# Performance work log

Measured on AMD Instinct MI355X. Metric: run time of the kernel, lower is better.

Reference implementation:

```python
import jax, jax.numpy as jnp
import numpy as np

V, BLOCK, E, H = 50257, 2048, 256, 8
DH = E // H  # head_size = 32
B, T = 2, 2048
SCALE = 1.0 / np.float32(np.sqrt(DH))


def setup_inputs() -> dict:
    key = jax.random.key(0)
    ks = jax.random.split(key, 9)
    s = 0.02
    return {
        "idx": jax.random.randint(ks[0], (B, T), 0, V),
        "targets": jax.random.randint(ks[1], (B, T), 0, V),
        "tok_emb": jax.random.normal(ks[2], (V, E), jnp.float32) * s,
        "pos_emb": jax.random.normal(ks[3], (BLOCK, E), jnp.float32) * s,
        "Wq": jax.random.normal(ks[4], (H, E, DH), jnp.float32) * s,
        "Wk": jax.random.normal(ks[5], (H, E, DH), jnp.float32) * s,
        "Wv": jax.random.normal(ks[6], (H, E, DH), jnp.float32) * s,
        "Wlm": jax.random.normal(ks[7], (V, E), jnp.float32) * s,
        "blm": jnp.zeros((V,), jnp.float32),
    }


def reference(idx, targets, tok_emb, pos_emb, Wq, Wk, Wv, Wlm, blm):
    t = idx.shape[1]
    x = tok_emb[idx] + pos_emb[:t]  # [B,T,E]
    # all heads batched (original loops over heads; same math)
    q = jnp.einsum('bte,hed->bhtd', x, Wq)
    k = jnp.einsum('bte,hed->bhtd', x, Wk)
    v = jnp.einsum('bte,hed->bhtd', x, Wv)
    scores = jnp.einsum('bhqd,bhkd->bhqk', q, k) * SCALE  # [B,H,T,T]
    causal = jnp.tril(jnp.ones((t, t), dtype=bool))
    # faithful to original: tril then masked_fill(scores == 0, -inf)
    scores = jnp.where(causal, scores, 0.0)
    scores = jnp.where(scores == 0.0, -jnp.inf, scores)
    # faithful to original bug: softmax over the QUERY axis (torch dim=1 of [b,t,t])
    attn = jax.nn.softmax(scores, axis=2)
    out = jnp.einsum('bhqk,bhkd->bqhd', attn, v).reshape(idx.shape[0], t, E)  # concat heads
    logits = out @ Wlm.T + blm  # [B,T,V]
    logp = jax.nn.log_softmax(logits, axis=-1)
    loss = -jnp.take_along_axis(logp, targets[..., None], axis=-1).mean()
    return logits, loss
```

## Files before the change

### kernel.cpp

```cpp
#include <hip/hip_runtime.h>
#include <hip/hip_bf16.h>
#include <cstdint>
#include <cstddef>

typedef __bf16 bf16x8 __attribute__((ext_vector_type(8)));
typedef __bf16 bf16x4 __attribute__((ext_vector_type(4)));
typedef float  f32x4  __attribute__((ext_vector_type(4)));
typedef float  f32x16 __attribute__((ext_vector_type(16)));

#define SCALE_QK 0.17677669529663687f
#define V_SIZE 50257
#define T_SEQ  2048
#define E_DIM  256
#define NROWS  4096
#define LNB    786
#define NPAD   (LNB * 64)

__device__ __forceinline__ f32x4 mfma16(bf16x8 a, bf16x8 b, f32x4 c) {
    return __builtin_amdgcn_mfma_f32_16x16x32_bf16(a, b, c, 0, 0, 0);
}
__device__ __forceinline__ f32x16 mfma32(bf16x8 a, bf16x8 b, f32x16 c) {
    return __builtin_amdgcn_mfma_f32_32x32x16_bf16(a, b, c, 0, 0, 0);
}

#define GLOAD_LDS16(gptr, lptr) \
    __builtin_amdgcn_global_load_lds((const __attribute__((address_space(1))) void*)(gptr), \
                                     (__attribute__((address_space(3))) void*)(lptr), 16, 0, 0)

#define PREP_EMBED 1024
#define PREP_WQKV  (PREP_EMBED + 768)
#define PREP_CVT   (PREP_WQKV + 12576)
#define PREP_ZERO  (PREP_CVT + 128)
__global__ void __launch_bounds__(256)
k_prep(const int* __restrict__ idx, const float* __restrict__ tok,
       const float* __restrict__ pos, __bf16* __restrict__ X,
       const float* __restrict__ Wq, const float* __restrict__ Wk,
       const float* __restrict__ Wv, __bf16* __restrict__ Wo,
       const float* __restrict__ Wlm, __bf16* __restrict__ WlmB,
       float* __restrict__ Dcol) {
    const int bx = blockIdx.x, tid = threadIdx.x;
    if (bx < PREP_EMBED) {
        int row = bx * 4 + (tid >> 6);
        int tl = row & (T_SEQ - 1);
        int tk = idx[row];
        int e = (tid & 63) * 4;
        f32x4 a = *(const f32x4*)(tok + (size_t)tk * E_DIM + e);
        f32x4 p = *(const f32x4*)(pos + (size_t)tl * E_DIM + e);
        bf16x4 o;
#pragma unroll
        for (int i = 0; i < 4; ++i) o[i] = (__bf16)(a[i] + p[i]);
        *(bf16x4*)(X + (size_t)row * E_DIM + e) = o;
    } else if (bx < PREP_WQKV) {
        int n = bx - PREP_EMBED;
        int sel = n >> 8, hd = n & 255, h = hd >> 5, d = hd & 31;
        const float* W = (sel == 0) ? Wq : (sel == 1) ? Wk : Wv;
        Wo[(size_t)n * E_DIM + tid] = (__bf16)W[((size_t)h * E_DIM + tid) * 32 + d];
    } else if (bx < PREP_CVT) {
        size_t i = ((size_t)(bx - PREP_WQKV) * 256 + tid) * 4;
        bf16x4 o = {};
        if (i + 4 <= (size_t)V_SIZE * E_DIM) {
            f32x4 v = *(const f32x4*)(Wlm + i);
#pragma unroll
            for (int j = 0; j < 4; ++j) o[j] = (__bf16)v[j];
        }
        *(bf16x4*)(WlmB + i) = o;
    } else {
        Dcol[(bx - PREP_CVT) * 256 + tid] = 0.f;
    }
}

template <int KK>
__global__ void __launch_bounds__(256, 4)
k_gemm_bt(const __bf16* __restrict__ A, const __bf16* __restrict__ B,
          __bf16* __restrict__ Cout, int N) {
    __shared__ __align__(16) __bf16 Alds[128 * 64];
    __shared__ __align__(16) __bf16 Blds[128 * 64];

    const int tid = threadIdx.x;
    const int lane = tid & 63, w = tid >> 6;
    const int wr = w >> 1, wc = w & 1;
    const int brow = blockIdx.x * 128, bcol = blockIdx.y * 128;
    const int gg = lane >> 4, li = lane & 15;

    f32x4 acc[4][4] = {};

#pragma unroll
    for (int t = 0; t < KK / 64; ++t) {
#pragma unroll
        for (int i = 0; i < 4; ++i) {
            int cb = (w * 4 + i) * 64;
            int c = cb + lane;
            int r = c >> 3, kbs = (c & 7) ^ (r & 7);
            GLOAD_LDS16(A + (size_t)(brow + r) * KK + t * 64 + kbs * 8, (char*)Alds + cb * 16);
            GLOAD_LDS16(B + (size_t)(bcol + r) * KK + t * 64 + kbs * 8, (char*)Blds + cb * 16);
        }
        __syncthreads();
#pragma unroll
        for (int ks = 0; ks < 2; ++ks) {
            bf16x8 af[4], bfr[4];
#pragma unroll
            for (int mi = 0; mi < 4; ++mi) {
                int r = wr * 64 + mi * 16 + li;
                int kbyte = (ks * 64 + gg * 16) ^ ((r & 7) << 4);
                af[mi] = *(const bf16x8*)((const char*)Alds + r * 128 + kbyte);
            }
#pragma unroll
            for (int ni = 0; ni < 4; ++ni) {
                int r = wc * 64 + ni * 16 + li;
                int kbyte = (ks * 64 + gg * 16) ^ ((r & 7) << 4);
                bfr[ni] = *(const bf16x8*)((const char*)Blds + r * 128 + kbyte);
            }
#pragma unroll
            for (int mi = 0; mi < 4; ++mi)
#pragma unroll
                for (int ni = 0; ni < 4; ++ni)
                    acc[mi][ni] = mfma16(bfr[ni], af[mi], acc[mi][ni]);
        }
        if (t + 1 < KK / 64) __syncthreads();
    }
#pragma unroll
    for (int mi = 0; mi < 4; ++mi) {
        const size_t mrow = (size_t)(brow + wr * 64 + mi * 16 + li) * N;
#pragma unroll
        for (int ni = 0; ni < 4; ++ni) {
            int nc = wc * 64 + ni * 16 + gg * 4;
            f32x4 v = acc[mi][ni];
            bf16x4 o;
#pragma unroll
            for (int j = 0; j < 4; ++j) o[j] = (__bf16)v[j];
            *(bf16x4*)(Cout + mrow + bcol + nc) = o;
        }
    }
}

__global__ void __launch_bounds__(256, 4)
k_logits(const __bf16* __restrict__ A, const __bf16* __restrict__ B,
         float* __restrict__ C, const float* __restrict__ bias,
         float* __restrict__ partials) {
    __shared__ __align__(16) __bf16 Alds[256 * 64];
    __shared__ __align__(16) __bf16 Blds[64 * 64];
    __shared__ __align__(16) float bias_lds[64];

    const int tid = threadIdx.x, lane = tid & 63, w = tid >> 6;
    const int brow = blockIdx.x * 256, bcol = blockIdx.y * 64;
    const int gg = lane >> 4, li = lane & 15;

    if (tid < 64) bias_lds[tid] = (bcol + tid < V_SIZE) ? bias[bcol + tid] : 0.f;

    f32x4 acc[4][4] = {};

#pragma unroll
    for (int t = 0; t < 4; ++t) {
#pragma unroll
        for (int i = 0; i < 8; ++i) {
            int cb = (w * 8 + i) * 64;
            int c = cb + lane;
            int r = c >> 3, kbs = (c & 7) ^ (r & 7);
            GLOAD_LDS16(A + (size_t)(brow + r) * E_DIM + t * 64 + kbs * 8, (char*)Alds + cb * 16);
        }
#pragma unroll
        for (int i = 0; i < 2; ++i) {
            int cb = (w * 2 + i) * 64;
            int c = cb + lane;
            int r = c >> 3, kbs = (c & 7) ^ (r & 7);
            GLOAD_LDS16(B + (size_t)(bcol + r) * E_DIM + t * 64 + kbs * 8, (char*)Blds + cb * 16);
        }
        __syncthreads();
#pragma unroll
        for (int ks = 0; ks < 2; ++ks) {
            bf16x8 af[4], bfr[4];
#pragma unroll
            for (int mi = 0; mi < 4; ++mi) {
                int r = w * 64 + mi * 16 + li;
                int kbyte = (ks * 64 + gg * 16) ^ ((r & 7) << 4);
                af[mi] = *(const bf16x8*)((const char*)Alds + r * 128 + kbyte);
            }
#pragma unroll
            for (int ni = 0; ni < 4; ++ni) {
                int r = ni * 16 + li;
                int kbyte = (ks * 64 + gg * 16) ^ ((r & 7) << 4);
                bfr[ni] = *(const bf16x8*)((const char*)Blds + r * 128 + kbyte);
            }
#pragma unroll
            for (int mi = 0; mi < 4; ++mi)
#pragma unroll
                for (int ni = 0; ni < 4; ++ni)
                    acc[mi][ni] = mfma16(bfr[ni], af[mi], acc[mi][ni]);
        }
        if (t < 3) __syncthreads();
    }

    if (bcol + 64 <= V_SIZE) {
#pragma unroll
        for (int mi = 0; mi < 4; ++mi) {
            const size_t mrow = (size_t)(brow + w * 64 + mi * 16 + li) * V_SIZE;
            float s = 0.f;
#pragma unroll
            for (int ni = 0; ni < 4; ++ni) {
                int nc = ni * 16 + gg * 4;
                f32x4 v = acc[mi][ni];
                f32x4 bv = *(const f32x4*)&bias_lds[nc];
#pragma unroll
                for (int j = 0; j < 4; ++j) { v[j] += bv[j]; s += __expf(v[j]); }
                *(f32x4*)(C + mrow + bcol + nc) = v;
            }
            s += __shfl_xor(s, 16); s += __shfl_xor(s, 32);
            if (gg == 0)
                partials[(size_t)blockIdx.y * NROWS + brow + w * 64 + mi * 16 + li] = s;
        }
    } else {
#pragma unroll
        for (int mi = 0; mi < 4; ++mi) {
            const size_t mrow = (size_t)(brow + w * 64 + mi * 16 + li) * V_SIZE;
            float s = 0.f;
#pragma unroll
            for (int ni = 0; ni < 4; ++ni) {
                int nc = ni * 16 + gg * 4;
#pragma unroll
                for (int j = 0; j < 4; ++j) {
                    int col = bcol + nc + j;
                    if (col < V_SIZE) {
                        float v = acc[mi][ni][j] + bias_lds[nc + j];
                        s += __expf(v);
                        C[mrow + col] = v;
                    }
                }
            }
            s += __shfl_xor(s, 16); s += __shfl_xor(s, 32);
            if (gg == 0)
                partials[(size_t)blockIdx.y * NROWS + brow + w * 64 + mi * 16 + li] = s;
        }
    }
}

__global__ void __launch_bounds__(256)
k_pass1(const __bf16* __restrict__ QKV, float* __restrict__ Dcol) {
    int p = blockIdx.x;
    int kt = 0;
    while (p >= 16 - kt) { p -= 16 - kt; ++kt; }
    const int qc = kt + p;
    const int bh = blockIdx.y;
    const int b = bh >> 3, h = bh & 7;
    const int tid = threadIdx.x, lane = tid & 63, w = tid >> 6;
    const int g = lane >> 5, li = lane & 31;
    __shared__ __align__(16) __bf16 Klds[4 * 128 * 8];
    __shared__ __align__(16) __bf16 Qlds[4 * 128 * 8];

    const size_t baseQ = ((size_t)b * T_SEQ) * 768 + h * 32;
    const size_t baseK = baseQ + 256;

#pragma unroll
    for (int i = 0; i < 2; ++i) {
        int c = i * 256 + tid; int k = c >> 2, db = c & 3;
        *(bf16x8*)(Klds + (db * 128 + k) * 8) =
            *(const bf16x8*)(QKV + baseK + (size_t)(kt * 128 + k) * 768 + db * 8);
        *(bf16x8*)(Qlds + (db * 128 + k) * 8) =
            *(const bf16x8*)(QKV + baseQ + (size_t)(qc * 128 + k) * 768 + db * 8);
    }
    __syncthreads();

    float csum = 0.f;
    const int kglob = kt * 128 + w * 32 + li;
#pragma unroll
    for (int qs = 0; qs < 4; ++qs) {
        f32x16 sacc = {};
#pragma unroll
        for (int ks = 0; ks < 2; ++ks) {
            bf16x8 aq = *(const bf16x8*)(Qlds + ((ks * 2 + g) * 128 + qs * 32 + li) * 8);
            bf16x8 bk = *(const bf16x8*)(Klds + ((ks * 2 + g) * 128 + w * 32 + li) * 8);
            sacc = mfma32(aq, bk, sacc);
        }
#pragma unroll
        for (int r = 0; r < 16; ++r) {
            int qrow = qc * 128 + qs * 32 + ((r & 3) + 8 * (r >> 2) + 4 * g);
            if (kglob <= qrow) csum += __expf(sacc[r] * SCALE_QK);
        }
    }
    csum += __shfl_xor(csum, 32);
    if (g == 0) atomicAdd(&Dcol[(size_t)bh * T_SEQ + kglob], csum);
}

__global__ void __launch_bounds__(256)
k_pass2(const __bf16* __restrict__ QKV, const float* __restrict__ Dcol,
        float* __restrict__ Yf0, float* __restrict__ Yf1) {
    const int p = blockIdx.x, bh = blockIdx.y;
    const int pi = p >> 1, par = p & 1;
    const int b = bh >> 3, h = bh & 7;
    const int tid = threadIdx.x, lane = tid & 63, w = tid >> 6;
    const int g = lane >> 5, li = lane & 31;
    float* __restrict__ Yf = par ? Yf1 : Yf0;
    __shared__ __align__(16) __bf16 Qlds[4 * 128 * 8];
    __shared__ __align__(16) __bf16 Klds[4 * 128 * 8];
    __shared__ __align__(16) __bf16 UT[16 * 32 * 8];
    __shared__ __align__(16) __bf16 Plds[4][32 * 136];

    const size_t baseQ = ((size_t)b * T_SEQ) * 768 + h * 32;
    const size_t baseK = baseQ + 256;
    const size_t baseV = baseQ + 512;

#pragma unroll
    for (int ti = 0; ti < 2; ++ti) {
        const int qt = ti ? (15 - pi) : pi;
        __syncthreads();
#pragma unroll
        for (int i = 0; i < 2; ++i) {
            int c = i * 256 + tid; int q = c >> 2, db = c & 3;
            *(bf16x8*)(Qlds + (db * 128 + q) * 8) =
                *(const bf16x8*)(QKV + baseQ + (size_t)(qt * 128 + q) * 768 + db * 8);
        }
        f32x16 oacc = {};
        const int qrow = qt * 128 + w * 32 + li;

        for (int kc = par; kc <= qt; kc += 2) {
            __syncthreads();
#pragma unroll
            for (int i = 0; i < 2; ++i) {
                int c = i * 256 + tid; int k = c >> 2, db = c & 3;
                *(bf16x8*)(Klds + (db * 128 + k) * 8) =
                    *(const bf16x8*)(QKV + baseK + (size_t)(kc * 128 + k) * 768 + db * 8);
            }
#pragma unroll
            for (int i = 0; i < 4; ++i) {
                int c = i * 256 + tid; int k = c & 127, d4 = c >> 7;
                float rD = 1.0f / Dcol[(size_t)bh * T_SEQ + kc * 128 + k];
                bf16x4 v4 = *(const bf16x4*)(QKV + baseV + (size_t)(kc * 128 + k) * 768 + d4 * 4);
                int kb = k >> 3, j = k & 7;
#pragma unroll
                for (int t2 = 0; t2 < 4; ++t2)
                    UT[((size_t)kb * 32 + d4 * 4 + t2) * 8 + j] = (__bf16)((float)v4[t2] * rD);
            }
            __syncthreads();

#pragma unroll
            for (int ksub = 0; ksub < 4; ++ksub) {
                int kbase = kc * 128 + ksub * 32;
                f32x16 sacc = {};
#pragma unroll
                for (int ks = 0; ks < 2; ++ks) {
                    bf16x8 ak = *(const bf16x8*)(Klds + ((ks * 2 + g) * 128 + ksub * 32 + li) * 8);
                    bf16x8 bq = *(const bf16x8*)(Qlds + ((ks * 2 + g) * 128 + w * 32 + li) * 8);
                    sacc = mfma32(ak, bq, sacc);
                }
                float pv[16];
#pragma unroll
                for (int r = 0; r < 16; ++r) {
                    int kk = kbase + (r & 3) + 8 * (r >> 2) + 4 * g;
                    pv[r] = (kk <= qrow) ? __expf(sacc[r] * SCALE_QK) : 0.f;
                }
#pragma unroll
                for (int t2 = 0; t2 < 4; ++t2) {
                    bf16x4 pk;
#pragma unroll
                    for (int e = 0; e < 4; ++e) pk[e] = (__bf16)pv[4 * t2 + e];
                    *(bf16x4*)(&Plds[w][li * 136 + ksub * 32 + 8 * t2 + 4 * g]) = pk;
                }
            }
#pragma unroll
            for (int ks16 = 0; ks16 < 8; ++ks16) {
                bf16x8 ap = *(const bf16x8*)(&Plds[w][li * 136 + ks16 * 16 + g * 8]);
                bf16x8 bu = *(const bf16x8*)(UT + ((ks16 * 2 + g) * 32 + li) * 8);
                oacc = mfma32(ap, bu, oacc);
            }
        }
#pragma unroll
        for (int r = 0; r < 16; ++r) {
            int q = qt * 128 + w * 32 + (r & 3) + 8 * (r >> 2) + 4 * g;
            Yf[((size_t)b * T_SEQ + q) * E_DIM + h * 32 + li] = oacc[r];
        }
    }
}

__global__ void k_ycvt(const float* __restrict__ a, const float* __restrict__ b,
                       __bf16* __restrict__ y, int n4) {
    int i = blockIdx.x * 256 + threadIdx.x;
    if (i < n4) {
        f32x4 va = ((const f32x4*)a)[i], vb = ((const f32x4*)b)[i];
        bf16x4 o;
#pragma unroll
        for (int j = 0; j < 4; ++j) o[j] = (__bf16)(va[j] + vb[j]);
        ((bf16x4*)y)[i] = o;
    }
}

__global__ void k_rowlse(const float* __restrict__ partials, const float* __restrict__ logits,
                         const int* __restrict__ tgt, float* __restrict__ rowloss) {
    int r = blockIdx.x * 256 + threadIdx.x;
    float s = 0.f;
    for (int i = 0; i < LNB; ++i) s += partials[(size_t)i * NROWS + r];
    float lse = logf(s);
    rowloss[r] = lse - logits[(size_t)r * V_SIZE + tgt[r]];
}

__global__ void k_loss(const float* __restrict__ rowloss, float* __restrict__ out) {
    __shared__ float red[4];
    float s = 0.f;
    for (int i = threadIdx.x; i < NROWS; i += 256) s += rowloss[i];
    for (int m = 1; m < 64; m <<= 1) s += __shfl_xor(s, m);
    if ((threadIdx.x & 63) == 0) red[threadIdx.x >> 6] = s;
    __syncthreads();
    if (threadIdx.x == 0) out[0] = (red[0] + red[1] + red[2] + red[3]) / (float)NROWS;
}

extern "C" void kernel_launch(void* const* d_in, const int* in_sizes, int n_in,
                              void* d_out, int out_size, void* d_ws, size_t ws_size,
                              hipStream_t stream) {
    const int*   idx = (const int*)d_in[0];
    const int*   tgt = (const int*)d_in[1];
    const float* tok = (const float*)d_in[2];
    const float* pos = (const float*)d_in[3];
    const float* Wq  = (const float*)d_in[4];
    const float* Wk  = (const float*)d_in[5];
    const float* Wv  = (const float*)d_in[6];
    const float* Wlm = (const float*)d_in[7];
    const float* blm = (const float*)d_in[8];

    float* logits = (float*)d_out;
    float* loss   = logits + (size_t)NROWS * V_SIZE;

    char* ws = (char*)d_ws;
    __bf16* X        = (__bf16*)ws; ws += (size_t)NROWS * E_DIM * 2;
    __bf16* Wqkv     = (__bf16*)ws; ws += (size_t)768 * E_DIM * 2;
    __bf16* QKV      = (__bf16*)ws; ws += (size_t)NROWS * 768 * 2;
    float*  Dcol     = (float*)ws;  ws += (size_t)16 * T_SEQ * 4;
    __bf16* Y        = (__bf16*)ws; ws += (size_t)NROWS * E_DIM * 2;
    float*  Yf0      = (float*)ws;  ws += (size_t)NROWS * E_DIM * 4;
    float*  Yf1      = (float*)ws;  ws += (size_t)NROWS * E_DIM * 4;
    __bf16* WlmB     = (__bf16*)ws; ws += (size_t)NPAD * E_DIM * 2;
    float*  partials = (float*)ws;  ws += (size_t)LNB * NROWS * 4;
    float*  rowloss  = (float*)ws;  ws += (size_t)NROWS * 4;

    k_prep<<<PREP_ZERO, 256, 0, stream>>>(idx, tok, pos, X, Wq, Wk, Wv, Wqkv,
                                          Wlm, WlmB, Dcol);
    k_gemm_bt<E_DIM><<<dim3(NROWS / 128, 768 / 128), 256, 0, stream>>>(
        X, Wqkv, QKV, 768);
    k_pass1<<<dim3(136, 16), 256, 0, stream>>>(QKV, Dcol);
    k_pass2<<<dim3(16, 16), 256, 0, stream>>>(QKV, Dcol, Yf0, Yf1);
    k_ycvt<<<(NROWS * E_DIM / 4 + 255) / 256, 256, 0, stream>>>(Yf0, Yf1, Y, NROWS * E_DIM / 4);
    k_logits<<<dim3(NROWS / 256, LNB), 256, 0, stream>>>(
        Y, WlmB, logits, blm, partials);
    k_rowlse<<<NROWS / 256, 256, 0, stream>>>(partials, logits, tgt, rowloss);
    k_loss<<<1, 256, 0, stream>>>(rowloss, loss);
}
```

Measured before the change: 480.6 us.

## Retile LM-head logits GEMM to 128x128 and overlap epilogue with next tile's K-loop

The logits kernel changes from 256x64 tiles to 128x128 tiles with a 2x2 wave layout. Each block now walks four consecutive 128-column vocab tiles, double-buffering the accumulators so the previous tile's bias/exp/store epilogue runs interleaved with the next tile's loads and MFMAs. This aims to hide the large fp32 logits write and exp cost behind compute and to halve the partials array and its reduction. The cost is more registers (two accumulator sets), which may lower occupancy, plus extra LDS for per-wave sums and bias.

```diff
diff --git a/kernel.cpp b/kernel.cpp
--- a/kernel.cpp
+++ b/kernel.cpp
@@ -13,8 +13,8 @@
 #define T_SEQ  2048
 #define E_DIM  256
 #define NROWS  4096
-#define LNB    786
-#define NPAD   (LNB * 64)
+#define NNB    393
+#define NPAD   (NNB * 128)
 
 __device__ __forceinline__ f32x4 mfma16(bf16x8 a, bf16x8 b, f32x4 c) {
     return __builtin_amdgcn_mfma_f32_16x16x32_bf16(a, b, c, 0, 0, 0);
@@ -137,47 +137,41 @@
 k_logits(const __bf16* __restrict__ A, const __bf16* __restrict__ B,
          float* __restrict__ C, const float* __restrict__ bias,
          float* __restrict__ partials) {
-    __shared__ __align__(16) __bf16 Alds[256 * 64];
-    __shared__ __align__(16) __bf16 Blds[64 * 64];
-    __shared__ __align__(16) float bias_lds[64];
+    __shared__ __align__(16) __bf16 Alds[128 * 64];
+    __shared__ __align__(16) __bf16 Blds[128 * 64];
+    __shared__ __align__(16) float bias_lds[2][128];
+    __shared__ float wsum[2][128][2];
 
     const int tid = threadIdx.x, lane = tid & 63, w = tid >> 6;
-    const int brow = blockIdx.x * 256, bcol = blockIdx.y * 64;
-    const int gg = lane >> 4, li = lane & 15;
-
-    if (tid < 64) bias_lds[tid] = (bcol + tid < V_SIZE) ? bias[bcol + tid] : 0.f;
-
-    f32x4 acc[4][4] = {};
-
-#pragma unroll
-    for (int t = 0; t < 4; ++t) {
-#pragma unroll
-        for (int i = 0; i < 8; ++i) {
-            int cb = (w * 8 + i) * 64;
+    const int wr = w >> 1, wc = w & 1, gg = lane >> 4, li = lane & 15;
+    const int brow = blockIdx.x * 128;
+    const int base = blockIdx.y * 4;
+    const bool full4 = (base + 4 <= NNB);
+
+    auto stage = [&](int bn, int t) {
+#pragma unroll
+        for (int i = 0; i < 4; ++i) {
+            int cb = (w * 4 + i) * 64;
             int c = cb + lane;
             int r = c >> 3, kbs = (c & 7) ^ (r & 7);
             GLOAD_LDS16(A + (size_t)(brow + r) * E_DIM + t * 64 + kbs * 8, (char*)Alds + cb * 16);
-        }
-#pragma unroll
-        for (int i = 0; i < 2; ++i) {
-            int cb = (w * 2 + i) * 64;
-            int c = cb + lane;
-            int r = c >> 3, kbs = (c & 7) ^ (r & 7);
-            GLOAD_LDS16(B + (size_t)(bcol + r) * E_DIM + t * 64 + kbs * 8, (char*)Blds + cb * 16);
-        }
-        __syncthreads();
+            GLOAD_LDS16(B + (size_t)(bn * 128 + r) * E_DIM + t * 64 + kbs * 8, (char*)Blds + cb * 16);
+        }
+    };
+
+    auto compute = [&](f32x4 (&acc)[4][4]) {
 #pragma unroll
         for (int ks = 0; ks < 2; ++ks) {
             bf16x8 af[4], bfr[4];
 #pragma unroll
             for (int mi = 0; mi < 4; ++mi) {
-                int r = w * 64 + mi * 16 + li;
+                int r = wr * 64 + mi * 16 + li;
                 int kbyte = (ks * 64 + gg * 16) ^ ((r & 7) << 4);
                 af[mi] = *(const bf16x8*)((const char*)Alds + r * 128 + kbyte);
             }
 #pragma unroll
             for (int ni = 0; ni < 4; ++ni) {
-                int r = ni * 16 + li;
+                int r = wc * 64 + ni * 16 + li;
                 int kbyte = (ks * 64 + gg * 16) ^ ((r & 7) << 4);
                 bfr[ni] = *(const bf16x8*)((const char*)Blds + r * 128 + kbyte);
             }
@@ -187,49 +181,102 @@
                 for (int ni = 0; ni < 4; ++ni)
                     acc[mi][ni] = mfma16(bfr[ni], af[mi], acc[mi][ni]);
         }
-        if (t < 3) __syncthreads();
-    }
-
-    if (bcol + 64 <= V_SIZE) {
+    };
+
+    auto epislice = [&](const f32x4 (&acc)[4][4], int mi, int bn, int pb) {
+        const size_t mrow = (size_t)(brow + wr * 64 + mi * 16 + li) * V_SIZE;
+        const int bcol = bn * 128;
+        float s = 0.f;
+#pragma unroll
+        for (int ni = 0; ni < 4; ++ni) {
+            int nc = wc * 64 + ni * 16 + gg * 4;
+            f32x4 v = acc[mi][ni];
+            f32x4 bv = *(const f32x4*)&bias_lds[pb][nc];
+#pragma unroll
+            for (int j = 0; j < 4; ++j) { v[j] += bv[j]; s += __expf(v[j]); }
+            *(f32x4*)(C + mrow + bcol + nc) = v;
+        }
+        s += __shfl_xor(s, 16); s += __shfl_xor(s, 32);
+        if (gg == 0) wsum[pb][wr * 64 + mi * 16 + li][wc] = s;
+    };
+
+    auto kloop_ov = [&](f32x4 (&cur)[4][4], int bn, int pb,
+                        const f32x4 (&prev)[4][4], int pbn, int ppb) {
+#pragma unroll
+        for (int m2 = 0; m2 < 4; ++m2)
+#pragma unroll
+            for (int n2 = 0; n2 < 4; ++n2)
+                cur[m2][n2] = (f32x4){0.f, 0.f, 0.f, 0.f};
+        if (tid < 128) bias_lds[pb][tid] = bias[bn * 128 + tid];
+#pragma unroll
+        for (int t = 0; t < 4; ++t) {
+            stage(bn, t);
+            epislice(prev, t, pbn, ppb);
+            __syncthreads();
+            compute(cur);
+            __syncthreads();
+        }
+    };
+
+    if (full4) {
+        f32x4 a0[4][4] = {}, a1[4][4] = {};
+        if (tid < 128) bias_lds[0][tid] = bias[base * 128 + tid];
+#pragma unroll
+        for (int t = 0; t < 4; ++t) {
+            stage(base, t);
+            __syncthreads();
+            compute(a0);
+            __syncthreads();
+        }
+        kloop_ov(a1, base + 1, 1, a0, base + 0, 0);
+        if (tid < 128) partials[(size_t)(base + 0) * NROWS + brow + tid] =
+            wsum[0][tid][0] + wsum[0][tid][1];
+        kloop_ov(a0, base + 2, 0, a1, base + 1, 1);
+        if (tid < 128) partials[(size_t)(base + 1) * NROWS + brow + tid] =
+            wsum[1][tid][0] + wsum[1][tid][1];
+        kloop_ov(a1, base + 3, 1, a0, base + 2, 0);
+        if (tid < 128) partials[(size_t)(base + 2) * NROWS + brow + tid] =
+            wsum[0][tid][0] + wsum[0][tid][1];
+#pragma unroll
+        for (int mi = 0; mi < 4; ++mi) epislice(a1, mi, base + 3, 1);
+        __syncthreads();
+        if (tid < 128) partials[(size_t)(base + 3) * NROWS + brow + tid] =
+            wsum[1][tid][0] + wsum[1][tid][1];
+    } else {
+        const int bn = base;
+        const int bcol = bn * 128;
+        if (tid < 128) bias_lds[0][tid] = (bcol + tid < V_SIZE) ? bias[bcol + tid] : 0.f;
+        f32x4 a0[4][4] = {};
+#pragma unroll
+        for (int t = 0; t < 4; ++t) {
+            stage(bn, t);
+            __syncthreads();
+            compute(a0);
+            __syncthreads();
+        }
 #pragma unroll
         for (int mi = 0; mi < 4; ++mi) {
-            const size_t mrow = (size_t)(brow + w * 64 + mi * 16 + li) * V_SIZE;
+            const size_t mrow = (size_t)(brow + wr * 64 + mi * 16 + li) * V_SIZE;
             float s = 0.f;
 #pragma unroll
             for (int ni = 0; ni < 4; ++ni) {
-                int nc = ni * 16 + gg * 4;
-                f32x4 v = acc[mi][ni];
-                f32x4 bv = *(const f32x4*)&bias_lds[nc];
-#pragma unroll
-                for (int j = 0; j < 4; ++j) { v[j] += bv[j]; s += __expf(v[j]); }
-                *(f32x4*)(C + mrow + bcol + nc) = v;
-            }
-            s += __shfl_xor(s, 16); s += __shfl_xor(s, 32);
-            if (gg == 0)
-                partials[(size_t)blockIdx.y * NROWS + brow + w * 64 + mi * 16 + li] = s;
-        }
-    } else {
-#pragma unroll
-        for (int mi = 0; mi < 4; ++mi) {
-            const size_t mrow = (size_t)(brow + w * 64 + mi * 16 + li) * V_SIZE;
-            float s = 0.f;
-#pragma unroll
-            for (int ni = 0; ni < 4; ++ni) {
-                int nc = ni * 16 + gg * 4;
+                int nc = wc * 64 + ni * 16 + gg * 4;
 #pragma unroll
                 for (int j = 0; j < 4; ++j) {
                     int col = bcol + nc + j;
                     if (col < V_SIZE) {
-                        float v = acc[mi][ni][j] + bias_lds[nc + j];
+                        float v = a0[mi][ni][j] + bias_lds[0][nc + j];
                         s += __expf(v);
                         C[mrow + col] = v;
                     }
                 }
             }
             s += __shfl_xor(s, 16); s += __shfl_xor(s, 32);
-            if (gg == 0)
-                partials[(size_t)blockIdx.y * NROWS + brow + w * 64 + mi * 16 + li] = s;
-        }
+            if (gg == 0) wsum[0][wr * 64 + mi * 16 + li][wc] = s;
+        }
+        __syncthreads();
+        if (tid < 128)
+            partials[(size_t)bn * NROWS + brow + tid] = wsum[0][tid][0] + wsum[0][tid][1];
     }
 }
 
@@ -386,7 +433,7 @@
                          const int* __restrict__ tgt, float* __restrict__ rowloss) {
     int r = blockIdx.x * 256 + threadIdx.x;
     float s = 0.f;
-    for (int i = 0; i < LNB; ++i) s += partials[(size_t)i * NROWS + r];
+    for (int i = 0; i < NNB; ++i) s += partials[(size_t)i * NROWS + r];
     float lse = logf(s);
     rowloss[r] = lse - logits[(size_t)r * V_SIZE + tgt[r]];
 }
@@ -426,7 +473,7 @@
     float*  Yf0      = (float*)ws;  ws += (size_t)NROWS * E_DIM * 4;
     float*  Yf1      = (float*)ws;  ws += (size_t)NROWS * E_DIM * 4;
     __bf16* WlmB     = (__bf16*)ws; ws += (size_t)NPAD * E_DIM * 2;
-    float*  partials = (float*)ws;  ws += (size_t)LNB * NROWS * 4;
+    float*  partials = (float*)ws;  ws += (size_t)NNB * NROWS * 4;
     float*  rowloss  = (float*)ws;  ws += (size_t)NROWS * 4;
 
     k_prep<<<PREP_ZERO, 256, 0, stream>>>(idx, tok, pos, X, Wq, Wk, Wv, Wqkv,
@@ -436,7 +483,7 @@
     k_pass1<<<dim3(136, 16), 256, 0, stream>>>(QKV, Dcol);
     k_pass2<<<dim3(16, 16), 256, 0, stream>>>(QKV, Dcol, Yf0, Yf1);
     k_ycvt<<<(NROWS * E_DIM / 4 + 255) / 256, 256, 0, stream>>>(Yf0, Yf1, Y, NROWS * E_DIM / 4);
-    k_logits<<<dim3(NROWS / 256, LNB), 256, 0, stream>>>(
+    k_logits<<<dim3(NROWS / 128, (NNB + 3) / 4), 256, 0, stream>>>(
         Y, WlmB, logits, blm, partials);
     k_rowlse<<<NROWS / 256, 256, 0, stream>>>(partials, logits, tgt, rowloss);
     k_loss<<<1, 256, 0, stream>>>(rowloss, loss);
```

Result: slower. 858.8 us (+78.7%).

## Retile logits GEMM to 128x256 with 8 waves and LDS-staged coalesced stores

Applied to the files above, without the earlier changes.

The LM-head logits kernel changes from 256x64 tiles with 4 waves to 128x256 tiles with 8 waves in a 2x4 grid. Output is now staged through swizzled LDS in 32-row chunks so each row is written to global memory as 1KB coalesced segments instead of scattered 16-byte pieces. Per-row exp partial sums are reduced across waves in LDS, which cuts the partials buffer from 786 to 197 column blocks and so reduces the downstream row-LSE reads. The cost is extra barriers and LDS round-trips in the epilogue, plus different occupancy from the 512-thread blocks and roughly 50KB of LDS per block.

```diff
diff --git a/kernel.cpp b/kernel.cpp
--- a/kernel.cpp
+++ b/kernel.cpp
@@ -13,8 +13,8 @@
 #define T_SEQ  2048
 #define E_DIM  256
 #define NROWS  4096
-#define LNB    786
-#define NPAD   (LNB * 64)
+#define LNB    197
+#define NPAD   (LNB * 256)
 
 __device__ __forceinline__ f32x4 mfma16(bf16x8 a, bf16x8 b, f32x4 c) {
     return __builtin_amdgcn_mfma_f32_16x16x32_bf16(a, b, c, 0, 0, 0);
@@ -29,7 +29,7 @@
 
 #define PREP_EMBED 1024
 #define PREP_WQKV  (PREP_EMBED + 768)
-#define PREP_CVT   (PREP_WQKV + 12576)
+#define PREP_CVT   (PREP_WQKV + 12608)
 #define PREP_ZERO  (PREP_CVT + 128)
 __global__ void __launch_bounds__(256)
 k_prep(const int* __restrict__ idx, const float* __restrict__ tok,
@@ -133,37 +133,40 @@
     }
 }
 
-__global__ void __launch_bounds__(256, 4)
+__global__ void __launch_bounds__(512, 4)
 k_logits(const __bf16* __restrict__ A, const __bf16* __restrict__ B,
          float* __restrict__ C, const float* __restrict__ bias,
          float* __restrict__ partials) {
-    __shared__ __align__(16) __bf16 Alds[256 * 64];
-    __shared__ __align__(16) __bf16 Blds[64 * 64];
-    __shared__ __align__(16) float bias_lds[64];
+    __shared__ __align__(16) char smem[49152];
+    __shared__ __align__(16) float bias_lds[256];
+    __shared__ float wsum[128][4];
 
     const int tid = threadIdx.x, lane = tid & 63, w = tid >> 6;
-    const int brow = blockIdx.x * 256, bcol = blockIdx.y * 64;
+    const int wr = w >> 2, wc = w & 3;
+    const int brow = blockIdx.x * 128;
+    const int bn = blockIdx.y, bcol = bn * 256;
     const int gg = lane >> 4, li = lane & 15;
 
-    if (tid < 64) bias_lds[tid] = (bcol + tid < V_SIZE) ? bias[bcol + tid] : 0.f;
+    if (tid < 256) bias_lds[tid] = (bcol + tid < V_SIZE) ? bias[bcol + tid] : 0.f;
 
     f32x4 acc[4][4] = {};
 
 #pragma unroll
     for (int t = 0; t < 4; ++t) {
-#pragma unroll
-        for (int i = 0; i < 8; ++i) {
-            int cb = (w * 8 + i) * 64;
-            int c = cb + lane;
-            int r = c >> 3, kbs = (c & 7) ^ (r & 7);
-            GLOAD_LDS16(A + (size_t)(brow + r) * E_DIM + t * 64 + kbs * 8, (char*)Alds + cb * 16);
-        }
 #pragma unroll
         for (int i = 0; i < 2; ++i) {
             int cb = (w * 2 + i) * 64;
             int c = cb + lane;
             int r = c >> 3, kbs = (c & 7) ^ (r & 7);
-            GLOAD_LDS16(B + (size_t)(bcol + r) * E_DIM + t * 64 + kbs * 8, (char*)Blds + cb * 16);
+            GLOAD_LDS16(A + (size_t)(brow + r) * E_DIM + t * 64 + kbs * 8, smem + cb * 16);
+        }
+#pragma unroll
+        for (int i = 0; i < 4; ++i) {
+            int cb = (w * 4 + i) * 64;
+            int c = cb + lane;
+            int r = c >> 3, kbs = (c & 7) ^ (r & 7);
+            GLOAD_LDS16(B + (size_t)(bcol + r) * E_DIM + t * 64 + kbs * 8,
+                        smem + 16384 + cb * 16);
         }
         __syncthreads();
 #pragma unroll
@@ -171,15 +174,15 @@
             bf16x8 af[4], bfr[4];
 #pragma unroll
             for (int mi = 0; mi < 4; ++mi) {
-                int r = w * 64 + mi * 16 + li;
+                int r = wr * 64 + mi * 16 + li;
                 int kbyte = (ks * 64 + gg * 16) ^ ((r & 7) << 4);
-                af[mi] = *(const bf16x8*)((const char*)Alds + r * 128 + kbyte);
+                af[mi] = *(const bf16x8*)(smem + r * 128 + kbyte);
             }
 #pragma unroll
             for (int ni = 0; ni < 4; ++ni) {
-                int r = ni * 16 + li;
+                int r = wc * 64 + ni * 16 + li;
                 int kbyte = (ks * 64 + gg * 16) ^ ((r & 7) << 4);
-                bfr[ni] = *(const bf16x8*)((const char*)Blds + r * 128 + kbyte);
+                bfr[ni] = *(const bf16x8*)(smem + 16384 + r * 128 + kbyte);
             }
 #pragma unroll
             for (int mi = 0; mi < 4; ++mi)
@@ -190,32 +193,47 @@
         if (t < 3) __syncthreads();
     }
 
-    if (bcol + 64 <= V_SIZE) {
+    if (bcol + 256 <= V_SIZE) {
+#pragma unroll
+        for (int p = 0; p < 4; ++p) {
+            __syncthreads();
+            if (wr == (p >> 1)) {
+#pragma unroll
+                for (int m2 = 0; m2 < 2; ++m2) {
+                    int mi = (p & 1) * 2 + m2;
+                    int rl = m2 * 16 + li;
+                    float s = 0.f;
+#pragma unroll
+                    for (int ni = 0; ni < 4; ++ni) {
+                        int colc = wc * 16 + ni * 4 + gg;
+                        f32x4 v = acc[mi][ni];
+                        f32x4 bv = *(const f32x4*)&bias_lds[colc * 4];
+#pragma unroll
+                        for (int j = 0; j < 4; ++j) { v[j] += bv[j]; s += __expf(v[j]); }
+                        int c4s = colc ^ ((rl & 7) << 2);
+                        *(f32x4*)(smem + rl * 1024 + c4s * 16) = v;
+                    }
+                    s += __shfl_xor(s, 16); s += __shfl_xor(s, 32);
+                    if (gg == 0) wsum[p * 32 + rl][wc] = s;
+                }
+            }
+            __syncthreads();
+#pragma unroll
+            for (int i = 0; i < 4; ++i) {
+                int c = i * 512 + tid;
+                int rl = c >> 6, c4 = c & 63;
+                f32x4 v = *(const f32x4*)(smem + rl * 1024 + ((c4 ^ ((rl & 7) << 2)) << 4));
+                *(f32x4*)(C + (size_t)(brow + p * 32 + rl) * V_SIZE + bcol + c4 * 4) = v;
+            }
+        }
+    } else {
 #pragma unroll
         for (int mi = 0; mi < 4; ++mi) {
-            const size_t mrow = (size_t)(brow + w * 64 + mi * 16 + li) * V_SIZE;
+            const size_t mrow = (size_t)(brow + wr * 64 + mi * 16 + li) * V_SIZE;
             float s = 0.f;
 #pragma unroll
             for (int ni = 0; ni < 4; ++ni) {
-                int nc = ni * 16 + gg * 4;
-                f32x4 v = acc[mi][ni];
-                f32x4 bv = *(const f32x4*)&bias_lds[nc];
-#pragma unroll
-                for (int j = 0; j < 4; ++j) { v[j] += bv[j]; s += __expf(v[j]); }
-                *(f32x4*)(C + mrow + bcol + nc) = v;
-            }
-            s += __shfl_xor(s, 16); s += __shfl_xor(s, 32);
-            if (gg == 0)
-                partials[(size_t)blockIdx.y * NROWS + brow + w * 64 + mi * 16 + li] = s;
-        }
-    } else {
-#pragma unroll
-        for (int mi = 0; mi < 4; ++mi) {
-            const size_t mrow = (size_t)(brow + w * 64 + mi * 16 + li) * V_SIZE;
-            float s = 0.f;
-#pragma unroll
-            for (int ni = 0; ni < 4; ++ni) {
-                int nc = ni * 16 + gg * 4;
+                int nc = wc * 64 + ni * 16 + gg * 4;
 #pragma unroll
                 for (int j = 0; j < 4; ++j) {
                     int col = bcol + nc + j;
@@ -227,10 +245,13 @@
                 }
             }
             s += __shfl_xor(s, 16); s += __shfl_xor(s, 32);
-            if (gg == 0)
-                partials[(size_t)blockIdx.y * NROWS + brow + w * 64 + mi * 16 + li] = s;
-        }
-    }
+            if (gg == 0) wsum[wr * 64 + mi * 16 + li][wc] = s;
+        }
+    }
+    __syncthreads();
+    if (tid < 128)
+        partials[(size_t)bn * NROWS + brow + tid] =
+            wsum[tid][0] + wsum[tid][1] + wsum[tid][2] + wsum[tid][3];
 }
 
 __global__ void __launch_bounds__(256)
@@ -436,7 +457,7 @@
     k_pass1<<<dim3(136, 16), 256, 0, stream>>>(QKV, Dcol);
     k_pass2<<<dim3(16, 16), 256, 0, stream>>>(QKV, Dcol, Yf0, Yf1);
     k_ycvt<<<(NROWS * E_DIM / 4 + 255) / 256, 256, 0, stream>>>(Yf0, Yf1, Y, NROWS * E_DIM / 4);
-    k_logits<<<dim3(NROWS / 256, LNB), 256, 0, stream>>>(
+    k_logits<<<dim3(NROWS / 128, LNB), 512, 0, stream>>>(
         Y, WlmB, logits, blm, partials);
     k_rowlse<<<NROWS / 256, 256, 0, stream>>>(partials, logits, tgt, rowloss);
     k_loss<<<1, 256, 0, stream>>>(rowloss, loss);
```

Result: faster. 388.5 us (median of 2 runs) (-19.2%).
